# Optimization experiments

Measured on AMD Instinct MI355X. Metric: run time of the kernel, lower is better.

The kernel has to match this reference:

```python
import jax, jax.numpy as jnp
import numpy as np

EPS = 1e-8  # torch F.cosine_similarity eps


def _mp_cos(p, q, w):
    # multi-perspective cosine: p,q (b,s,h), w (l,h) -> (b,s,l)
    pw = p[:, None, :, :] * w[None, :, None, :]   # (b,l,s,h)
    qw = q[:, None, :, :] * w[None, :, None, :]
    num = jnp.sum(pw * qw, axis=-1)
    den = jnp.maximum(jnp.linalg.norm(pw, axis=-1) * jnp.linalg.norm(qw, axis=-1), EPS)
    return (num / den).transpose(0, 2, 1)          # (b,s,l)


def _full(p, q, w, direction):
    # match every step of p against last (fw) / first (bw) step of q
    q_t = q[:, -1, :] if direction == 'fw' else q[:, 0, :]
    return _mp_cos(p, jnp.broadcast_to(q_t[:, None, :], p.shape), w)


def _maxpool(p, q, w):
    pw = p[:, None, :, :] * w[None, :, None, :]    # (b,l,sp,h)
    qw = q[:, None, :, :] * w[None, :, None, :]    # (b,l,sq,h)
    dot = jnp.einsum('blph,blqh->blpq', pw, qw)
    mag = jnp.linalg.norm(pw, axis=-1)[..., None] * jnp.linalg.norm(qw, axis=-1)[:, :, None, :]
    cos = (dot / mag).transpose(0, 2, 3, 1)        # (b,sp,sq,l)
    return cos.max(axis=2), cos.max(axis=1)        # (b,sp,l), (b,sq,l)


def _attentive(p, q, w, att):
    pn = jnp.linalg.norm(p, axis=2)                # (b,sp)
    qn = jnp.linalg.norm(q, axis=2)                # (b,sq)
    cos = jnp.einsum('bph,bqh->bpq', p, q) / (pn[:, :, None] * qn[:, None, :])
    if att == 'mean':
        # weighted sums without materializing (b,sp,sq,h)
        p_vec = jnp.einsum('bph,bpq->bqh', p, cos) / cos.sum(axis=1)[..., None]  # (b,sq,h)
        q_vec = jnp.einsum('bqh,bpq->bph', q, cos) / cos.sum(axis=2)[..., None]  # (b,sp,h)
    else:  # 'max' -- elementwise max requires the broadcasted tensor
        p_vec = (p[:, :, None, :] * cos[..., None]).max(axis=1)  # (b,sq,h)
        q_vec = (q[:, None, :, :] * cos[..., None]).max(axis=2)  # (b,sp,h)
    return _mp_cos(p, q_vec, w), _mp_cos(q, p_vec, w)


def _forward(p, q, W):
    h = W.shape[-1]
    pf, pb = p[..., :h], p[..., h:]
    qf, qb = q[..., :h], q[..., h:]
    mv_p, mv_q = [], []
    # full matching
    mv_p += [_full(pf, qf, W[0], 'fw'), _full(pb, qb, W[1], 'bw')]
    mv_q += [_full(qf, pf, W[0], 'fw'), _full(qb, pb, W[1], 'bw')]
    # maxpool matching
    pp_f, pq_f = _maxpool(pf, qf, W[2])
    pp_b, pq_b = _maxpool(pb, qb, W[3])
    mv_p += [pp_f, pp_b]
    mv_q += [pq_f, pq_b]
    # attentive (mean) matching
    ap_f, aq_f = _attentive(pf, qf, W[4], 'mean')
    ap_b, aq_b = _attentive(pb, qb, W[5], 'mean')
    mv_p += [ap_f, ap_b]
    mv_q += [aq_f, aq_b]
    # max-attentive matching
    mp_f, mq_f = _attentive(pf, qf, W[6], 'max')
    mp_b, mq_b = _attentive(pb, qb, W[7], 'max')
    mv_p += [mp_f, mp_b]
    mv_q += [mq_f, mq_b]
    # dropout is identity at inference (training=False)
    return jnp.concatenate(mv_p, axis=2), jnp.concatenate(mv_q, axis=2)


def setup_inputs() -> dict:
    key = jax.random.key(0)
    k1, k2, k3 = jax.random.split(key, 3)
    B, S, H, L = 32, 64, 300, 20
    p = jax.random.normal(k1, (B, S, 2 * H), dtype=jnp.float32)
    q = jax.random.normal(k2, (B, S, 2 * H), dtype=jnp.float32)
    W = jax.random.uniform(k3, (8, L, H), dtype=jnp.float32)  # torch.rand init
    return {"p": p, "q": q, "W": W}


def reference(p, q, W):
    return _forward(p, q, W)
```

## Files before the change

kernel.cpp:

```cpp
#include <hip/hip_runtime.h>

#define B_ 32
#define S_ 64
#define H_ 300
#define H2_ 600
#define L_ 20
#define ROW_ 160
#define OUTQ_OFF ((size_t)B_ * S_ * ROW_)
#define NEG_INF -3.402823466e38f

#define NB_COS 1024
#define NB_W 188
#define NB_MP 1280

typedef __attribute__((ext_vector_type(8))) _Float16 half8v;
typedef __attribute__((ext_vector_type(4))) _Float16 half4v;
typedef __attribute__((ext_vector_type(4))) float float4v;

struct CosS {
  float xq[S_][65];
  float xp[4][68];
  float qn_l[S_];
  float cp[4][S_];
};

__device__ __forceinline__ void cos_body(char* smem, int bid,
                                         const float* __restrict__ P,
                                         const float* __restrict__ Q,
                                         float* __restrict__ cosM,
                                         float* __restrict__ sumpart,
                                         float* __restrict__ sum_q) {
  CosS& S = *(CosS*)smem;
  int bd = bid >> 4, pg = bid & 15;
  int b = bd >> 1, dir = bd & 1;
  int t = threadIdx.x;
  int q = t & 63, pr = t >> 6;
  const float* Pb = P + (size_t)b * S_ * H2_ + dir * H_;
  const float* Qb = Q + (size_t)b * S_ * H2_ + dir * H_;
  float dot = 0.f, np2 = 0.f, nq2 = 0.f;
  for (int c0 = 0; c0 < H_; c0 += 64) {
    __syncthreads();
#pragma unroll
    for (int jj = 0; jj < 4; ++jj) {
      int idx = t + 256 * jj;
      int s = idx >> 4, g = idx & 15;
      int h = c0 + 4 * g;
      float4v v = {0.f, 0.f, 0.f, 0.f};
      if (h < 297) v = *(const float4v*)&Qb[(size_t)s * H2_ + h];
      S.xq[s][4 * g + 0] = v.x; S.xq[s][4 * g + 1] = v.y;
      S.xq[s][4 * g + 2] = v.z; S.xq[s][4 * g + 3] = v.w;
    }
    if (t < 64) {
      int s = t >> 4, g = t & 15;
      int h = c0 + 4 * g;
      float4v v = {0.f, 0.f, 0.f, 0.f};
      if (h < 297) v = *(const float4v*)&Pb[(size_t)(pg * 4 + s) * H2_ + h];
      *(float4v*)&S.xp[s][4 * g] = v;
    }
    __syncthreads();
    for (int hh = 0; hh < 64; hh += 4) {
      float4v av = *(const float4v*)&S.xp[pr][hh];
      float q0 = S.xq[q][hh + 0];
      float q1 = S.xq[q][hh + 1];
      float q2 = S.xq[q][hh + 2];
      float q3 = S.xq[q][hh + 3];
      dot = fmaf(av.x, q0, dot); dot = fmaf(av.y, q1, dot);
      dot = fmaf(av.z, q2, dot); dot = fmaf(av.w, q3, dot);
      np2 = fmaf(av.x, av.x, np2); np2 = fmaf(av.y, av.y, np2);
      np2 = fmaf(av.z, av.z, np2); np2 = fmaf(av.w, av.w, np2);
      if (pr == 0) {
        nq2 = fmaf(q0, q0, nq2); nq2 = fmaf(q1, q1, nq2);
        nq2 = fmaf(q2, q2, nq2); nq2 = fmaf(q3, q3, nq2);
      }
    }
  }
  if (pr == 0) S.qn_l[q] = sqrtf(nq2);
  __syncthreads();
  float pn = sqrtf(np2);
  float c = dot / (pn * S.qn_l[q]);
  int p = pg * 4 + pr;
  cosM[(size_t)bd * S_ * S_ + (size_t)p * S_ + q] = c;
  float rs = c;
#pragma unroll
  for (int m = 1; m < 64; m <<= 1) rs += __shfl_xor(rs, m);
  if (q == 0) sum_q[bd * S_ + p] = rs;
  S.cp[pr][q] = c;
  __syncthreads();
  if (t < S_)
    sumpart[((size_t)bd * 16 + pg) * S_ + t] =
        S.cp[0][t] + S.cp[1][t] + S.cp[2][t] + S.cp[3][t];
}

#define HP 72
struct MaxpoolS {
  _Float16 ph[S_][HP];
  _Float16 qh[S_][HP];
  float w1s[H_];
  float pn2[S_], qn2[S_];
  float colp[4][S_];
};

__device__ __forceinline__ void maxpool_body(char* smem, int bid,
                                             const float* __restrict__ P,
                                             const float* __restrict__ Q,
                                             const float* __restrict__ Wf,
                                             float* __restrict__ out) {
  MaxpoolS& S = *(MaxpoolS*)smem;
  int x = bid & 7, j = bid >> 3;
  int bd = x + 8 * (j & 7);
  int l = j >> 3;
  int b = bd >> 1, dir = bd & 1;
  int t = threadIdx.x;
  int w = t >> 6, lane = t & 63, quad = lane >> 4, col = lane & 15;
  const float* wg = Wf + (size_t)(2 + dir) * L_ * H_ + (size_t)l * H_;
  if (t < 75) {
    float4v v = *(const float4v*)&wg[4 * t];
    float4v a = {fabsf(v.x), fabsf(v.y), fabsf(v.z), fabsf(v.w)};
    *(float4v*)&S.w1s[4 * t] = a;
  }
  const float* Pb = P + (size_t)b * S_ * H2_ + dir * H_;
  const float* Qb = Q + (size_t)b * S_ * H2_ + dir * H_;
  float4v acc[4];
#pragma unroll
  for (int qt = 0; qt < 4; ++qt) acc[qt] = (float4v){0.f, 0.f, 0.f, 0.f};
  float np2a[4] = {0.f, 0.f, 0.f, 0.f};
  float nq2a[4] = {0.f, 0.f, 0.f, 0.f};
  for (int h0 = 0; h0 < H_; h0 += 64) {
    __syncthreads();
#pragma unroll
    for (int jj = 0; jj < 4; ++jj) {
      int idx = t + 256 * jj;
      int s = idx >> 4, c4 = idx & 15;
      int h = h0 + 4 * c4;
      float4v pv = {0.f, 0.f, 0.f, 0.f}, qv = {0.f, 0.f, 0.f, 0.f};
      if (h < 297) {
        float4v wv = *(const float4v*)&S.w1s[h];
        float4v p4 = *(const float4v*)&Pb[(size_t)s * H2_ + h];
        float4v q4 = *(const float4v*)&Qb[(size_t)s * H2_ + h];
        pv = p4 * wv;
        qv = q4 * wv;
      }
      half4v phv = __builtin_convertvector(pv, half4v);
      half4v qhv = __builtin_convertvector(qv, half4v);
      *(half4v*)&S.ph[s][4 * c4] = phv;
      *(half4v*)&S.qh[s][4 * c4] = qhv;
      float4v pf = __builtin_convertvector(phv, float4v);
      float4v qf = __builtin_convertvector(qhv, float4v);
      np2a[jj] += pf.x * pf.x + pf.y * pf.y + pf.z * pf.z + pf.w * pf.w;
      nq2a[jj] += qf.x * qf.x + qf.y * qf.y + qf.z * qf.z + qf.w * qf.w;
    }
    __syncthreads();
#pragma unroll
    for (int ks = 0; ks < 2; ++ks) {
      half8v ah = *(const half8v*)&S.ph[16 * w + col][ks * 32 + quad * 8];
#pragma unroll
      for (int qt = 0; qt < 4; ++qt) {
        half8v bh = *(const half8v*)&S.qh[16 * qt + col][ks * 32 + quad * 8];
        acc[qt] = __builtin_amdgcn_mfma_f32_16x16x32_f16(ah, bh, acc[qt], 0, 0, 0);
      }
    }
  }
#pragma unroll
  for (int jj = 0; jj < 4; ++jj) {
    float a = np2a[jj], bb = nq2a[jj];
#pragma unroll
    for (int m = 1; m < 16; m <<= 1) {
      a += __shfl_xor(a, m);
      bb += __shfl_xor(bb, m);
    }
    if ((t & 15) == 0) {
      int s = (t >> 4) + 16 * jj;
      S.pn2[s] = a;
      S.qn2[s] = bb;
    }
  }
  __syncthreads();
  float pnv[4];
#pragma unroll
  for (int r = 0; r < 4; ++r) pnv[r] = sqrtf(S.pn2[16 * w + quad * 4 + r]);
  float rowm[4] = {NEG_INF, NEG_INF, NEG_INF, NEG_INF};
#pragma unroll
  for (int qt = 0; qt < 4; ++qt) {
    float qnv = sqrtf(S.qn2[16 * qt + col]);
    float cmv = NEG_INF;
#pragma unroll
    for (int r = 0; r < 4; ++r) {
      float c = acc[qt][r] / (pnv[r] * qnv);
      rowm[r] = fmaxf(rowm[r], c);
      cmv = fmaxf(cmv, c);
    }
    cmv = fmaxf(cmv, __shfl_xor(cmv, 16));
    cmv = fmaxf(cmv, __shfl_xor(cmv, 32));
    if (quad == 0) S.colp[w][16 * qt + col] = cmv;
  }
#pragma unroll
  for (int m = 1; m < 16; m <<= 1)
#pragma unroll
    for (int r = 0; r < 4; ++r) rowm[r] = fmaxf(rowm[r], __shfl_xor(rowm[r], m));
  if (col == 0) {
#pragma unroll
    for (int r = 0; r < 4; ++r) {
      int p = 16 * w + quad * 4 + r;
      out[((size_t)b * S_ + p) * ROW_ + (2 + dir) * L_ + l] = rowm[r];
    }
  }
  __syncthreads();
  if (t < S_) {
    float m0 = fmaxf(fmaxf(S.colp[0][t], S.colp[1][t]), fmaxf(S.colp[2][t], S.colp[3][t]));
    out[OUTQ_OFF + ((size_t)b * S_ + t) * ROW_ + (2 + dir) * L_ + l] = m0;
  }
}

__global__ __launch_bounds__(256) void k1(const float* __restrict__ P,
                                          const float* __restrict__ Q,
                                          const float* __restrict__ Wf,
                                          float* __restrict__ w2r,
                                          float* __restrict__ cosM,
                                          float* __restrict__ sumpart,
                                          float* __restrict__ sum_q,
                                          float* __restrict__ out) {
  extern __shared__ char smem[];
  int bid = blockIdx.x;
  if (bid < NB_COS) {
    cos_body(smem, bid, P, Q, cosM, sumpart, sum_q);
  } else if (bid < NB_COS + NB_W) {
    int i = (bid - NB_COS) * 256 + threadIdx.x;
    if (i < 8 * L_ * H_) {
      float v = Wf[i];
      w2r[i] = v * v;
    }
  } else {
    maxpool_body(smem, bid - (NB_COS + NB_W), P, Q, Wf, out);
  }
}

#define SG 4
struct OutsS {
  float u[600];
  float xP[SG][H_], xQ[SG][H_];
  float vmq[SG][H_], vmp[SG][H_], vxq[SG][H_], vxp[SG][H_];
  float sps[SG], sqs[SG];
};

__global__ __launch_bounds__(256) void k2(const float* __restrict__ P,
                                          const float* __restrict__ Q,
                                          const float* __restrict__ w2r,
                                          const float* __restrict__ cosM,
                                          const float* __restrict__ sumpart,
                                          const float* __restrict__ sum_q,
                                          float* __restrict__ out) {
  extern __shared__ char smem[];
  OutsS& S = *(OutsS*)smem;
  int bid = blockIdx.x;
  int x = bid & 7, j = bid >> 3;
  int bd = x + 8 * (j & 7);
  int sg = j >> 3;
  int s0 = sg * SG;
  int b = bd >> 1, dir = bd & 1;
  int t = threadIdx.x;
  float (*cosT)[8] = (float (*)[8])&S.u[0];
  const float* cm = cosM + (size_t)bd * S_ * S_;
  for (int idx = t; idx < S_ * 8; idx += 256) {
    int k = idx >> 3, jj = idx & 7, si = jj & 3;
    cosT[k][jj] = (jj < 4) ? cm[(size_t)k * S_ + s0 + si]
                           : cm[(size_t)(s0 + si) * S_ + k];
  }
  if (t < SG) {
    float a = 0.f;
    for (int pg = 0; pg < 16; ++pg) a += sumpart[((size_t)bd * 16 + pg) * S_ + s0 + t];
    S.sps[t] = a;
    S.sqs[t] = sum_q[bd * S_ + s0 + t];
  }
  int tgt = dir ? 0 : S_ - 1;
  const float* Pb = P + (size_t)b * S_ * H2_ + dir * H_;
  const float* Qb = Q + (size_t)b * S_ * H2_ + dir * H_;
  for (int g = t; g < SG * 75; g += 256) {
    int si = g / 75, c4 = g - si * 75;
    *(float4v*)&S.xP[si][4 * c4] = *(const float4v*)&Pb[(size_t)(s0 + si) * H2_ + 4 * c4];
    *(float4v*)&S.xQ[si][4 * c4] = *(const float4v*)&Qb[(size_t)(s0 + si) * H2_ + 4 * c4];
  }
  __syncthreads();
  for (int h = t; h < H_; h += 256) {
    float amp[SG], amq[SG], axp[SG], axq[SG];
#pragma unroll
    for (int si = 0; si < SG; ++si) { amp[si] = 0.f; amq[si] = 0.f; axp[si] = NEG_INF; axq[si] = NEG_INF; }
    for (int k = 0; k < S_; k += 2) {
      float pv0 = Pb[(size_t)k * H2_ + h];
      float qv0 = Qb[(size_t)k * H2_ + h];
      float pv1 = Pb[(size_t)(k + 1) * H2_ + h];
      float qv1 = Qb[(size_t)(k + 1) * H2_ + h];
      float4v cc0 = *(const float4v*)&cosT[k][0];
      float4v cr0 = *(const float4v*)&cosT[k][4];
      float4v cc1 = *(const float4v*)&cosT[k + 1][0];
      float4v cr1 = *(const float4v*)&cosT[k + 1][4];
#pragma unroll
      for (int si = 0; si < SG; ++si) {
        float t1 = pv0 * cc0[si];
        amp[si] += t1; axp[si] = fmaxf(axp[si], t1);
        float t2 = qv0 * cr0[si];
        amq[si] += t2; axq[si] = fmaxf(axq[si], t2);
        float t3 = pv1 * cc1[si];
        amp[si] += t3; axp[si] = fmaxf(axp[si], t3);
        float t4 = qv1 * cr1[si];
        amq[si] += t4; axq[si] = fmaxf(axq[si], t4);
      }
    }
#pragma unroll
    for (int si = 0; si < SG; ++si) {
      S.vmq[si][h] = amq[si] / S.sqs[si];
      S.vmp[si][h] = amp[si] / S.sps[si];
      S.vxq[si][h] = axq[si];
      S.vxp[si][h] = axp[si];
    }
  }
  __syncthreads();
  float* tq = &S.u[0];
  float* tp = &S.u[300];
  if (t < 75) {
    *(float4v*)&tq[4 * t] = *(const float4v*)&Qb[(size_t)tgt * H2_ + 4 * t];
    *(float4v*)&tp[4 * t] = *(const float4v*)&Pb[(size_t)tgt * H2_ + 4 * t];
  }
  __syncthreads();
  const int wb_[6] = {0, 0, 4, 4, 6, 6};
#pragma unroll
  for (int r = 0; r < 2; ++r) {
    int job = t + 256 * r;
    if (job < 480) {
      int l = job / 24;
      int g = job - l * 24;
      int pr = g >> 2, si = g & 3;
      const float* xv = (pr & 1) ? S.xQ[si] : S.xP[si];
      const float* y;
      if (pr == 0) y = tq;
      else if (pr == 1) y = tp;
      else if (pr == 2) y = S.vmq[si];
      else if (pr == 3) y = S.vmp[si];
      else if (pr == 4) y = S.vxq[si];
      else y = S.vxp[si];
      int widx = wb_[pr] + dir;
      const float* wp = w2r + (size_t)widx * (L_ * H_) + (size_t)l * H_;
      float a1 = 0.f, a2 = 0.f, a3 = 0.f;
      for (int h4 = 0; h4 < H_; h4 += 4) {
        float4v wv = *(const float4v*)&wp[h4];
        float4v xx = *(const float4v*)&xv[h4];
        float4v yy = *(const float4v*)&y[h4];
#pragma unroll
        for (int jj = 0; jj < 4; ++jj) {
          float wx = wv[jj] * xx[jj];
          a1 = fmaf(wx, yy[jj], a1);
          a2 = fmaf(wx, xx[jj], a2);
          a3 = fmaf(wv[jj] * yy[jj], yy[jj], a3);
        }
      }
      float den = fmaxf(sqrtf(a2) * sqrtf(a3), 1e-8f);
      float c = a1 / den;
      int s = s0 + si;
      size_t base = ((pr & 1) ? OUTQ_OFF : 0) + ((size_t)b * S_ + s) * ROW_;
      out[base + (size_t)widx * L_ + l] = c;
    }
  }
}

extern "C" void kernel_launch(void* const* d_in, const int* in_sizes, int n_in,
                              void* d_out, int out_size, void* d_ws, size_t ws_size,
                              hipStream_t stream) {
  (void)out_size; (void)ws_size;
  int iw = 2;
  for (int i = 0; i < n_in; ++i) if (in_sizes[i] == 8 * L_ * H_) iw = i;
  int io[2] = {0, 1}, k = 0;
  for (int i = 0; i < n_in && k < 2; ++i) if (i != iw) io[k++] = i;
  const float* P  = (const float*)d_in[io[0]];
  const float* Q  = (const float*)d_in[io[1]];
  const float* Wf = (const float*)d_in[iw];
  float* out = (float*)d_out;

  float* ws = (float*)d_ws;
  float* w2r     = ws;
  float* cosM    = w2r + 48000;
  float* sumpart = cosM + 262144;
  float* sum_q   = sumpart + 65536;

  size_t sh1 = sizeof(CosS) > sizeof(MaxpoolS) ? sizeof(CosS) : sizeof(MaxpoolS);
  k1<<<NB_COS + NB_W + NB_MP, 256, sh1, stream>>>(P, Q, Wf, w2r, cosM, sumpart, sum_q, out);
  k2<<<B_ * 2 * 16, 256, sizeof(OutsS), stream>>>(P, Q, w2r, cosM, sumpart, sum_q, out);
}
```

Measured before the change: 141.1 us.

## Move maxpool blocks into second kernel interleaved with output blocks

Rebalances work across the two launches: the first kernel now only computes the cosine matrix and squared weights, while the second kernel runs maxpool blocks interleaved 5:4 with the attentive-output blocks. The intent is to shorten the first kernel's critical path and to let the independent maxpool work fill the second kernel alongside the dependent output work. Shared memory for the second kernel is sized to the larger of the two structs, which may lower occupancy for output blocks.

```diff
diff --git a/kernel.cpp b/kernel.cpp
--- a/kernel.cpp
+++ b/kernel.cpp
@@ -12,6 +12,7 @@
 #define NB_COS 1024
 #define NB_W 188
 #define NB_MP 1280
+#define NB_OUT 1024
 
 typedef __attribute__((ext_vector_type(8))) _Float16 half8v;
 typedef __attribute__((ext_vector_type(4))) _Float16 half4v;
@@ -211,29 +212,6 @@
   }
 }
 
-__global__ __launch_bounds__(256) void k1(const float* __restrict__ P,
-                                          const float* __restrict__ Q,
-                                          const float* __restrict__ Wf,
-                                          float* __restrict__ w2r,
-                                          float* __restrict__ cosM,
-                                          float* __restrict__ sumpart,
-                                          float* __restrict__ sum_q,
-                                          float* __restrict__ out) {
-  extern __shared__ char smem[];
-  int bid = blockIdx.x;
-  if (bid < NB_COS) {
-    cos_body(smem, bid, P, Q, cosM, sumpart, sum_q);
-  } else if (bid < NB_COS + NB_W) {
-    int i = (bid - NB_COS) * 256 + threadIdx.x;
-    if (i < 8 * L_ * H_) {
-      float v = Wf[i];
-      w2r[i] = v * v;
-    }
-  } else {
-    maxpool_body(smem, bid - (NB_COS + NB_W), P, Q, Wf, out);
-  }
-}
-
 #define SG 4
 struct OutsS {
   float u[600];
@@ -242,16 +220,15 @@
   float sps[SG], sqs[SG];
 };
 
-__global__ __launch_bounds__(256) void k2(const float* __restrict__ P,
+__device__ __forceinline__ void outs_body(char* smem, int bid,
+                                          const float* __restrict__ P,
                                           const float* __restrict__ Q,
                                           const float* __restrict__ w2r,
                                           const float* __restrict__ cosM,
                                           const float* __restrict__ sumpart,
                                           const float* __restrict__ sum_q,
                                           float* __restrict__ out) {
-  extern __shared__ char smem[];
   OutsS& S = *(OutsS*)smem;
-  int bid = blockIdx.x;
   int x = bid & 7, j = bid >> 3;
   int bd = x + 8 * (j & 7);
   int sg = j >> 3;
@@ -361,6 +338,44 @@
   }
 }
 
+__global__ __launch_bounds__(256) void kA(const float* __restrict__ P,
+                                          const float* __restrict__ Q,
+                                          const float* __restrict__ Wf,
+                                          float* __restrict__ w2r,
+                                          float* __restrict__ cosM,
+                                          float* __restrict__ sumpart,
+                                          float* __restrict__ sum_q) {
+  extern __shared__ char smem[];
+  int bid = blockIdx.x;
+  if (bid < NB_COS) {
+    cos_body(smem, bid, P, Q, cosM, sumpart, sum_q);
+  } else {
+    int i = (bid - NB_COS) * 256 + threadIdx.x;
+    if (i < 8 * L_ * H_) {
+      float v = Wf[i];
+      w2r[i] = v * v;
+    }
+  }
+}
+
+__global__ __launch_bounds__(256) void kB(const float* __restrict__ P,
+                                          const float* __restrict__ Q,
+                                          const float* __restrict__ Wf,
+                                          const float* __restrict__ w2r,
+                                          const float* __restrict__ cosM,
+                                          const float* __restrict__ sumpart,
+                                          const float* __restrict__ sum_q,
+                                          float* __restrict__ out) {
+  extern __shared__ char smem[];
+  int bid = blockIdx.x;
+  int grp = bid / 9, pos = bid - grp * 9;
+  if (pos < 5) {
+    maxpool_body(smem, grp * 5 + pos, P, Q, Wf, out);
+  } else {
+    outs_body(smem, grp * 4 + (pos - 5), P, Q, w2r, cosM, sumpart, sum_q, out);
+  }
+}
+
 extern "C" void kernel_launch(void* const* d_in, const int* in_sizes, int n_in,
                               void* d_out, int out_size, void* d_ws, size_t ws_size,
                               hipStream_t stream) {
@@ -380,7 +395,7 @@
   float* sumpart = cosM + 262144;
   float* sum_q   = sumpart + 65536;
 
-  size_t sh1 = sizeof(CosS) > sizeof(MaxpoolS) ? sizeof(CosS) : sizeof(MaxpoolS);
-  k1<<<NB_COS + NB_W + NB_MP, 256, sh1, stream>>>(P, Q, Wf, w2r, cosM, sumpart, sum_q, out);
-  k2<<<B_ * 2 * 16, 256, sizeof(OutsS), stream>>>(P, Q, w2r, cosM, sumpart, sum_q, out);
-}
+  size_t shB = sizeof(MaxpoolS) > sizeof(OutsS) ? sizeof(MaxpoolS) : sizeof(OutsS);
+  kA<<<NB_COS + NB_W, 256, sizeof(CosS), stream>>>(P, Q, Wf, w2r, cosM, sumpart, sum_q);
+  kB<<<NB_MP + NB_OUT, 256, shB, stream>>>(P, Q, Wf, w2r, cosM, sumpart, sum_q, out);
+}
```

New measurement: 168.2 us. 1.19x slower.
